# Kernel optimization log

Hardware: AMD Instinct MI355X
Metric: run time of the kernel (lower is better)

Reference implementation:

```python
import jax, jax.numpy as jnp
import numpy as np

N_POINTS = 2_097_152  # ~1448x1448 sample points
N_CELLS = 5
N_SHAPES = 3 * N_CELLS * N_CELLS  # 75 primitives (tri, circle, ellipse per cell)


def _build_params():
    # Replicates the structure of VectorGraphicsRGB2IntegrandSlang.__init__:
    # per cell: triangle (11 floats), circle (8 floats), ellipse (9 floats).
    rng = np.random.default_rng(42)
    n, jf = N_CELLS, 1.0
    cw = 1.0 / n
    params = []
    for i in range(n):
        for j in range(n):
            bx = (i + 0.5) / n + (rng.random() - 0.5) * jf * cw
            by = (j + 0.5) / n + (rng.random() - 0.5) * jf * cw
            rad = 0.4 / n
            ang = np.sort(rng.random(3) * 2.0 * 3.14159)
            pxs = np.clip(bx + rad * np.cos(ang), 0.0, 1.0)
            pys = np.clip(by + rad * np.sin(ang), 0.0, 1.0)
            params += [1.0, pxs[0], pys[0], pxs[1], pys[1], pxs[2], pys[2], 0.0] + list(rng.random(3))
            cxx = (i + 0.5) / n + (rng.random() - 0.5) * jf * cw
            cyy = (j + 0.5) / n + (rng.random() - 0.5) * jf * cw
            cr = rng.random() * 0.1 / n + 0.05 / n
            cxx = min(max(cxx, cr), 1.0 - cr)
            cyy = min(max(cyy, cr), 1.0 - cr)
            params += [3.0, cxx, cyy, cr, 0.0] + list(rng.random(3))
            exx = (i + 0.5) / n + (rng.random() - 0.5) * jf * cw
            eyy = (j + 0.5) / n + (rng.random() - 0.5) * jf * cw
            erx = rng.random() * 0.12 / n + 0.04 / n
            ery = rng.random() * 0.12 / n + 0.04 / n
            exx = min(max(exx, erx), 1.0 - erx)
            eyy = min(max(eyy, ery), 1.0 - ery)
            params += [2.0, exx, eyy, erx, ery, 0.0] + list(rng.random(3))
    return np.asarray(params, dtype=np.float32)  # [700]


def setup_inputs() -> dict:
    key = jax.random.key(0)
    k1, _ = jax.random.split(key)
    x = jax.random.uniform(k1, (N_POINTS, 2), dtype=jnp.float32)  # points in [0,1]^2
    p = jnp.asarray(_build_params())
    return {"x": x, "p": p}


def reference(x, p):
    # Parse the fixed-layout parameter vector: 25 cells x 28 floats.
    cells = p.reshape(N_CELLS * N_CELLS, 28)
    tri, circ, ell = cells[:, :11], cells[:, 11:19], cells[:, 19:]
    px, py = x[:, 0:1], x[:, 1:2]  # [N,1] broadcast against [25] shapes

    # Triangle containment: consistent sign of the three edge cross products.
    ax, ay, bx, by, cx, cy = (tri[:, k] for k in range(1, 7))
    e0 = (px - ax) * (by - ay) - (py - ay) * (bx - ax)  # [N,25]
    e1 = (px - bx) * (cy - by) - (py - by) * (cx - bx)
    e2 = (px - cx) * (ay - cy) - (py - cy) * (ax - cx)
    tri_in = ((e0 >= 0) & (e1 >= 0) & (e2 >= 0)) | ((e0 <= 0) & (e1 <= 0) & (e2 <= 0))

    # Circle containment.
    ocx, ocy, orr = circ[:, 1], circ[:, 2], circ[:, 3]
    circ_in = (px - ocx) ** 2 + (py - ocy) ** 2 <= orr ** 2

    # Ellipse containment.
    ecx, ecy, erx, ery = ell[:, 1], ell[:, 2], ell[:, 3], ell[:, 4]
    ell_in = ((px - ecx) / erx) ** 2 + ((py - ecy) / ery) ** 2 <= 1.0

    # Interleave per-cell in shader evaluation order: triangle, circle, ellipse.
    inside = jnp.stack([tri_in, circ_in, ell_in], axis=2).reshape(x.shape[0], N_SHAPES)
    colors = jnp.stack([tri[:, 8:11], circ[:, 5:8], ell[:, 6:9]], axis=1).reshape(N_SHAPES, 3)

    last = (N_SHAPES - 1) - jnp.argmax(inside[:, ::-1], axis=1)  # [N]
    any_in = inside.any(axis=1)
    return jnp.where(any_in[:, None], colors[last], jnp.zeros((), x.dtype))  # [N,3]
```

## Files before the change

kernel.cpp:

```cpp
#include <hip/hip_runtime.h>

#pragma clang fp contract(off)

#define NPTS 2097152
#define PPT  2
#define NTHREADS (NPTS / PPT)

#define L_COL  980
#define LDS_FLOATS (980 + 304)

#define EPS_T 1e-6f
#define EPS_C 1e-7f
#define EPS_E 1e-5f

__device__ __noinline__ int exact_point(float px, float py, int ih, int jh,
                                        const float* __restrict__ p) {
    int idx = -1;
#pragma clang loop unroll(disable)
    for (int s = 0; s < 4; ++s) {
        int ii = ih - 1 + (s >> 1), jj = jh - 1 + (s & 1);
        if ((unsigned)ii > 4u || (unsigned)jj > 4u) continue;
        int c = 5 * ii + jj;
        const float* cell = p + 28 * c;
        float ax = cell[1], ay = cell[2], bx = cell[3], by = cell[4], cx = cell[5], cy = cell[6];
        float e0 = (px - ax) * (by - ay) - (py - ay) * (bx - ax);
        float e1 = (px - bx) * (cy - by) - (py - by) * (cx - bx);
        float e2 = (px - cx) * (ay - cy) - (py - cy) * (ax - cx);
        bool tin = (e0 >= 0.f && e1 >= 0.f && e2 >= 0.f) ||
                   (e0 <= 0.f && e1 <= 0.f && e2 <= 0.f);
        if (tin) idx = 3 * c;
        float dx = px - cell[12], dy = py - cell[13];
        if (dx * dx + dy * dy <= cell[14] * cell[14]) idx = 3 * c + 1;
        float u = (px - cell[20]) / cell[22];
        float v = (py - cell[21]) / cell[23];
        if (u * u + v * v <= 1.0f) idx = 3 * c + 2;
    }
    return idx;
}

__global__ __launch_bounds__(256) void vg_fused(const float* __restrict__ x,
                                                const float* __restrict__ p,
                                                float* __restrict__ out) {
    __shared__ float lds[LDS_FLOATS];
    int tl = threadIdx.x;
    int t  = blockIdx.x * 256 + tl;

    if (tl < 49) {
        int gi = tl / 7, gj = tl % 7;
        float* o = lds + tl * 20;
        if (gi >= 1 && gi <= 5 && gj >= 1 && gj <= 5) {
            int c = (gi - 1) * 5 + (gj - 1);
            const float* cell = p + c * 28;
            float ax = cell[1], ay = cell[2], bx = cell[3], by = cell[4], cx = cell[5], cy = cell[6];
            float d0y = by - ay, d0x = bx - ax;
            float d1y = cy - by, d1x = cx - bx;
            float d2y = ay - cy, d2x = ax - cx;
            o[0] = d0y; o[1] = -d0x; o[2] = (float)((double)ay * (double)d0x - (double)ax * (double)d0y);
            o[3] = d1y; o[4] = -d1x; o[5] = (float)((double)by * (double)d1x - (double)bx * (double)d1y);
            o[6] = d2y; o[7] = -d2x; o[8] = (float)((double)cy * (double)d2x - (double)cx * (double)d2y);
            o[9]  = cell[12]; o[10] = cell[13]; o[11] = cell[14] * cell[14];
            o[12] = cell[20]; o[13] = cell[21]; o[14] = 1.0f / cell[22]; o[15] = 1.0f / cell[23];
        } else {
            o[0] = 0.f; o[1] = 0.f; o[2] = 10.f;
            o[3] = 0.f; o[4] = 0.f; o[5] = -10.f;
            o[6] = 0.f; o[7] = 0.f; o[8] = 0.f;
            o[9] = 0.f; o[10] = 0.f; o[11] = -10.f;
            o[12] = 1000.f; o[13] = 1000.f; o[14] = 1.f; o[15] = 1.f;
        }
        o[16] = 0.f; o[17] = 0.f; o[18] = 0.f; o[19] = 0.f;
    }
    if (tl >= 128 && tl < 204) {
        int e = tl - 128;
        float* col = lds + L_COL + e * 4;
        if (e < 75) {
            int c = e / 3, kind = e - 3 * c;
            const float* cell = p + c * 28;
            int base = (kind == 0) ? 8 : (kind == 1) ? 16 : 25;
            col[0] = cell[base]; col[1] = cell[base + 1]; col[2] = cell[base + 2];
        } else {
            col[0] = 0.f; col[1] = 0.f; col[2] = 0.f;
        }
        col[3] = 0.f;
    }
    __syncthreads();

    float4 xv = ((const float4*)x)[t];
    float PX[PPT] = {xv.x, xv.z};
    float PY[PPT] = {xv.y, xv.w};
    int idx[PPT], ih[PPT], jh[PPT];
    bool unc[PPT];

#pragma unroll
    for (int k = 0; k < PPT; ++k) {
        ih[k] = (int)floorf(__builtin_fmaf(PX[k], 5.0f, 0.4025f));
        jh[k] = (int)floorf(__builtin_fmaf(PY[k], 5.0f, 0.4025f));
        idx[k] = -1; unc[k] = false;
    }

#pragma unroll
    for (int k = 0; k < PPT; ++k) {
        float X = PX[k], Y = PY[k];
        const float* base = lds + (7 * ih[k] + jh[k]) * 20;
        float4 Q[4][4];
#pragma unroll
        for (int s = 0; s < 4; ++s) {
            const float4* c4 = (const float4*)(base + ((s >> 1) * 140 + (s & 1) * 20));
            Q[s][0] = c4[0]; Q[s][1] = c4[1]; Q[s][2] = c4[2]; Q[s][3] = c4[3];
        }

#pragma unroll
        for (int s = 0; s < 4; ++s) {
            float4 q0 = Q[s][0], q1 = Q[s][1], q2 = Q[s][2], q3 = Q[s][3];
            int gi = ih[k] + (s >> 1), gj = jh[k] + (s & 1);
            int sid = 15 * gi + 3 * gj - 18;

            float e0 = __builtin_fmaf(X, q0.x, __builtin_fmaf(Y, q0.y, q0.z));
            float e1 = __builtin_fmaf(X, q0.w, __builtin_fmaf(Y, q1.x, q1.y));
            float e2 = __builtin_fmaf(X, q1.z, __builtin_fmaf(Y, q1.w, q2.x));
            float lo = __builtin_fminf(__builtin_fminf(e0, e1), e2);
            float hi = __builtin_fmaxf(__builtin_fmaxf(e0, e1), e2);
            bool ts = (lo >= EPS_T) || (hi <= -EPS_T);
            bool tr = (lo >= -EPS_T) || (hi <= EPS_T);
            unc[k] = unc[k] | (ts != tr);
            idx[k] = ts ? sid : idx[k];

            float dx = X - q2.y, dy = Y - q2.z;
            float tc = __builtin_fmaf(dx, dx, dy * dy);
            unc[k] = unc[k] | (__builtin_fabsf(tc - q2.w) < EPS_C);
            idx[k] = (tc <= q2.w) ? sid + 1 : idx[k];

            float ex = X - q3.x, ey = Y - q3.y;
            float u = ex * q3.z, v = ey * q3.w;
            float te = __builtin_fmaf(u, u, v * v);
            unc[k] = unc[k] | (__builtin_fabsf(te - 1.0f) < EPS_E);
            idx[k] = (te <= 1.0f) ? sid + 2 : idx[k];
        }
    }

#pragma unroll
    for (int k = 0; k < PPT; ++k)
        if (__builtin_expect(unc[k], 0))
            idx[k] = exact_point(PX[k], PY[k], ih[k], jh[k], p);

    const float4* col4 = (const float4*)(lds + L_COL);
    float4 c0 = col4[idx[0] < 0 ? 75 : idx[0]];
    float4 c1 = col4[idx[1] < 0 ? 75 : idx[1]];

    float2* o2 = (float2*)out;
    o2[3 * t + 0] = make_float2(c0.x, c0.y);
    o2[3 * t + 1] = make_float2(c0.z, c1.x);
    o2[3 * t + 2] = make_float2(c1.y, c1.z);
}

extern "C" void kernel_launch(void* const* d_in, const int* in_sizes, int n_in,
                              void* d_out, int out_size, void* d_ws, size_t ws_size,
                              hipStream_t stream) {
    const float* x = (const float*)d_in[0];
    const float* p = (const float*)d_in[1];
    float* out = (float*)d_out;
    (void)d_ws; (void)ws_size;

    vg_fused<<<NTHREADS / 256, 256, 0, stream>>>(x, p, out);
}
```

Measured before the change: 80.40 us.

## Evaluate triangle and circle tests exactly in-kernel with SoA LDS layout

Replaces the precomputed edge-coefficient LDS table (20 floats per cell) with four structure-of-arrays float4 planes holding the raw vertices, circle and ellipse parameters. Triangle edge functions and circle distances are now computed the same way as the reference, so the epsilon uncertainty flags and exact-fallback checks for those shapes are removed. Only the ellipse test still falls back to the exact path. This trades a few extra subtractions per cell for fewer LDS loads and fewer fallback calls, and changes the padding sentinel values for out-of-range cells.

```diff
diff --git a/kernel.cpp b/kernel.cpp
--- a/kernel.cpp
+++ b/kernel.cpp
@@ -6,11 +6,12 @@
 #define PPT  2
 #define NTHREADS (NPTS / PPT)
 
-#define L_COL  980
-#define LDS_FLOATS (980 + 304)
+#define L_B    196
+#define L_C    392
+#define L_D    588
+#define L_COL  784
+#define LDS_FLOATS (784 + 304)
 
-#define EPS_T 1e-6f
-#define EPS_C 1e-7f
 #define EPS_E 1e-5f
 
 __device__ __noinline__ int exact_point(float px, float py, int ih, int jh,
@@ -47,27 +48,23 @@
 
     if (tl < 49) {
         int gi = tl / 7, gj = tl % 7;
-        float* o = lds + tl * 20;
+        float4* A = (float4*)lds;
+        float4* B = (float4*)(lds + L_B);
+        float4* C = (float4*)(lds + L_C);
+        float4* D = (float4*)(lds + L_D);
         if (gi >= 1 && gi <= 5 && gj >= 1 && gj <= 5) {
             int c = (gi - 1) * 5 + (gj - 1);
             const float* cell = p + c * 28;
-            float ax = cell[1], ay = cell[2], bx = cell[3], by = cell[4], cx = cell[5], cy = cell[6];
-            float d0y = by - ay, d0x = bx - ax;
-            float d1y = cy - by, d1x = cx - bx;
-            float d2y = ay - cy, d2x = ax - cx;
-            o[0] = d0y; o[1] = -d0x; o[2] = (float)((double)ay * (double)d0x - (double)ax * (double)d0y);
-            o[3] = d1y; o[4] = -d1x; o[5] = (float)((double)by * (double)d1x - (double)bx * (double)d1y);
-            o[6] = d2y; o[7] = -d2x; o[8] = (float)((double)cy * (double)d2x - (double)cx * (double)d2y);
-            o[9]  = cell[12]; o[10] = cell[13]; o[11] = cell[14] * cell[14];
-            o[12] = cell[20]; o[13] = cell[21]; o[14] = 1.0f / cell[22]; o[15] = 1.0f / cell[23];
+            A[tl] = make_float4(cell[1], cell[2], cell[3], cell[4]);
+            B[tl] = make_float4(cell[5], cell[6], cell[12], cell[13]);
+            C[tl] = make_float4(cell[14], cell[20], cell[21], 1.0f / cell[22]);
+            D[tl] = make_float4(1.0f / cell[23], 0.f, 0.f, 0.f);
         } else {
-            o[0] = 0.f; o[1] = 0.f; o[2] = 10.f;
-            o[3] = 0.f; o[4] = 0.f; o[5] = -10.f;
-            o[6] = 0.f; o[7] = 0.f; o[8] = 0.f;
-            o[9] = 0.f; o[10] = 0.f; o[11] = -10.f;
-            o[12] = 1000.f; o[13] = 1000.f; o[14] = 1.f; o[15] = 1.f;
+            A[tl] = make_float4(0.f, -2.f, 1.f, -2.f);
+            B[tl] = make_float4(0.f, -3.f, 50.f, 50.f);
+            C[tl] = make_float4(0.f, 50.f, 50.f, 1.f);
+            D[tl] = make_float4(1.f, 0.f, 0.f, 0.f);
         }
-        o[16] = 0.f; o[17] = 0.f; o[18] = 0.f; o[19] = 0.f;
     }
     if (tl >= 128 && tl < 204) {
         int e = tl - 128;
@@ -87,50 +84,53 @@
     float4 xv = ((const float4*)x)[t];
     float PX[PPT] = {xv.x, xv.z};
     float PY[PPT] = {xv.y, xv.w};
-    int idx[PPT], ih[PPT], jh[PPT];
+    int idx[PPT], ih[PPT], jh[PPT], sb[PPT], cb[PPT];
     bool unc[PPT];
 
 #pragma unroll
     for (int k = 0; k < PPT; ++k) {
         ih[k] = (int)floorf(__builtin_fmaf(PX[k], 5.0f, 0.4025f));
         jh[k] = (int)floorf(__builtin_fmaf(PY[k], 5.0f, 0.4025f));
+        cb[k] = 7 * ih[k] + jh[k];
+        sb[k] = 15 * ih[k] + 3 * jh[k] - 18;
         idx[k] = -1; unc[k] = false;
     }
+
+    const float4* LA = (const float4*)lds;
+    const float4* LB = (const float4*)(lds + L_B);
+    const float4* LC = (const float4*)(lds + L_C);
+    const int coff[4] = {0, 1, 7, 8};
+    const int soff[4] = {0, 3, 15, 18};
 
 #pragma unroll
     for (int k = 0; k < PPT; ++k) {
         float X = PX[k], Y = PY[k];
-        const float* base = lds + (7 * ih[k] + jh[k]) * 20;
-        float4 Q[4][4];
 #pragma unroll
         for (int s = 0; s < 4; ++s) {
-            const float4* c4 = (const float4*)(base + ((s >> 1) * 140 + (s & 1) * 20));
-            Q[s][0] = c4[0]; Q[s][1] = c4[1]; Q[s][2] = c4[2]; Q[s][3] = c4[3];
-        }
+            int ci = cb[k] + coff[s];
+            float4 A = LA[ci];
+            float4 B = LB[ci];
+            float4 C = LC[ci];
+            float iry = lds[L_D + 4 * ci];
+            int sid = sb[k] + soff[s];
 
-#pragma unroll
-        for (int s = 0; s < 4; ++s) {
-            float4 q0 = Q[s][0], q1 = Q[s][1], q2 = Q[s][2], q3 = Q[s][3];
-            int gi = ih[k] + (s >> 1), gj = jh[k] + (s & 1);
-            int sid = 15 * gi + 3 * gj - 18;
+            float d0y = A.w - A.y, d0x = A.z - A.x;
+            float d1y = B.y - A.w, d1x = B.x - A.z;
+            float d2y = A.y - B.y, d2x = A.x - B.x;
+            float e0 = (X - A.x) * d0y - (Y - A.y) * d0x;
+            float e1 = (X - A.z) * d1y - (Y - A.w) * d1x;
+            float e2 = (X - B.x) * d2y - (Y - B.y) * d2x;
+            bool tin = (e0 >= 0.f && e1 >= 0.f && e2 >= 0.f) ||
+                       (e0 <= 0.f && e1 <= 0.f && e2 <= 0.f);
+            idx[k] = tin ? sid : idx[k];
 
-            float e0 = __builtin_fmaf(X, q0.x, __builtin_fmaf(Y, q0.y, q0.z));
-            float e1 = __builtin_fmaf(X, q0.w, __builtin_fmaf(Y, q1.x, q1.y));
-            float e2 = __builtin_fmaf(X, q1.z, __builtin_fmaf(Y, q1.w, q2.x));
-            float lo = __builtin_fminf(__builtin_fminf(e0, e1), e2);
-            float hi = __builtin_fmaxf(__builtin_fmaxf(e0, e1), e2);
-            bool ts = (lo >= EPS_T) || (hi <= -EPS_T);
-            bool tr = (lo >= -EPS_T) || (hi <= EPS_T);
-            unc[k] = unc[k] | (ts != tr);
-            idx[k] = ts ? sid : idx[k];
+            float r2 = C.x * C.x;
+            float dx = X - B.z, dy = Y - B.w;
+            float tc = dx * dx + dy * dy;
+            idx[k] = (tc <= r2) ? sid + 1 : idx[k];
 
-            float dx = X - q2.y, dy = Y - q2.z;
-            float tc = __builtin_fmaf(dx, dx, dy * dy);
-            unc[k] = unc[k] | (__builtin_fabsf(tc - q2.w) < EPS_C);
-            idx[k] = (tc <= q2.w) ? sid + 1 : idx[k];
-
-            float ex = X - q3.x, ey = Y - q3.y;
-            float u = ex * q3.z, v = ey * q3.w;
+            float ex = X - C.y, ey = Y - C.z;
+            float u = ex * C.w, v = ey * iry;
             float te = __builtin_fmaf(u, u, v * v);
             unc[k] = unc[k] | (__builtin_fabsf(te - 1.0f) < EPS_E);
             idx[k] = (te <= 1.0f) ? sid + 2 : idx[k];
```

Result: no change. 79.33 us (median of 2 runs) (-1.3%).
